# Optimization experiments

Measured on AMD Instinct MI355X. Metric: run time of the kernel, lower is better.

The kernel has to match this reference:

```python
import jax, jax.numpy as jnp
import numpy as np
from jax import lax

B, NM, P, F, E, H, K = 32, 131072, 256, 3, 64, 4, 3
DH = E // H


def layer_norm(x, gamma, beta, eps=1e-5):
    mu = x.mean(-1, keepdims=True)
    var = ((x - mu) ** 2).mean(-1, keepdims=True)
    return (x - mu) * lax.rsqrt(var + eps) * gamma + beta


def knn_interp(x, pos_x, pos_y, k=K):
    """x: [B, Nx, F] features at pos_x [Nx, 2]; interpolate to pos_y [Ny, 2].
    Positions are shared across the batch (they are tiled in the torch code),
    so KNN indices/weights are computed once. Matches torch knn + inverse-
    squared-distance weighted scatter (uniform per-batch counts => gather form).
    """
    d2 = jnp.sum((pos_y[:, None, :] - pos_x[None, :, :]) ** 2, axis=-1)  # [Ny, Nx]
    neg_d2, idx = lax.top_k(-d2, k)                                      # [Ny, k]
    w = 1.0 / jnp.clip(-neg_d2, 1e-16)                                   # [Ny, k]
    w = lax.stop_gradient(w)  # torch computes weights under no_grad
    gathered = x[:, idx, :]                                              # [B, Ny, k, F]
    num = jnp.sum(gathered * w[None, :, :, None], axis=2)                # [B, Ny, F]
    den = jnp.sum(w, axis=1)[None, :, None]                              # [1, Ny, 1]
    return num / den


def setup_inputs() -> dict:
    key = jax.random.key(0)
    ks = jax.random.split(key, 8)
    return {
        "node_attr": jax.random.normal(ks[0], (B * NM, F), jnp.float32),
        "position_mesh": jax.random.uniform(ks[1], (NM, 2), jnp.float32),
        "position_pivotal": jax.random.uniform(ks[2], (P, 2), jnp.float32),
        "ln_gamma": jnp.ones((F,), jnp.float32),
        "ln_beta": jnp.zeros((F,), jnp.float32),
        "Wf": jax.random.normal(ks[3], (E, F), jnp.float32) * (2.0 / E) ** 0.5,
        "bf": jnp.zeros((E,), jnp.float32),
        "Wp": jax.random.normal(ks[4], (E, 2), jnp.float32) * (2.0 / E) ** 0.5,
        "bp": jnp.zeros((E,), jnp.float32),
        "in_proj_w": jax.random.normal(ks[5], (3 * E, E), jnp.float32) * (1.0 / E) ** 0.5,
        "in_proj_b": jnp.zeros((3 * E,), jnp.float32),
        "batch_size": B,
    }


def reference(node_attr, position_mesh, position_pivotal, ln_gamma, ln_beta,
              Wf, bf, Wp, bp, in_proj_w, in_proj_b, batch_size):
    x = node_attr.reshape(batch_size, -1, F)                 # [B, NM, F]
    # PivotalNorm after encoder (encoder/decoder MeshGraphNet omitted: undefined dep)
    x = layer_norm(x, ln_gamma, ln_beta)
    # ---- downsample: mesh -> pivotal via inverse-distance KNN interpolation ----
    y = knn_interp(x, position_mesh, position_pivotal)       # [B, P, F]
    # attention-based pooling over pivotal nodes
    q = (jnp.einsum('bpf,ef->bpe', y, Wf) + bf
         + (position_pivotal @ Wp.T + bp)[None])             # [B, P, E]
    Wq, Wk = in_proj_w[:E], in_proj_w[E:2 * E]
    bq, bk = in_proj_b[:E], in_proj_b[E:2 * E]
    Q = (q @ Wq.T + bq).reshape(batch_size, P, H, DH)
    Kt = (q @ Wk.T + bk).reshape(batch_size, P, H, DH)
    scores = jnp.einsum('bqhd,bkhd->bhqk', Q, Kt) / np.float32(np.sqrt(DH))
    attn = jax.nn.softmax(scores, axis=-1)                   # [B, H, P, P]
    attn_w = attn.mean(axis=1)                               # avg heads, [B, P, P]
    y = jnp.einsum('bqk,bkf->bqf', attn_w, y)                # [B, P, F]
    # ---- interpolate: pivotal -> mesh ----
    out = knn_interp(y, position_pivotal, position_mesh)     # [B, NM, F]
    return out.reshape(-1, F)
```

## Files before the change

### kernel.cpp

```cpp
#include <hip/hip_runtime.h>
#include <math.h>

#define NM 131072
#define PP 256
#define BB 32

#define CHUNKS 512
#define CHUNK_SZ 256

#define INF_F 3.0e38f
#define LDW 13

__device__ __forceinline__ void ins3(float d, int i,
    float& d0, float& d1, float& d2, int& i0, int& i1, int& i2) {
  bool l0 = d < d0, l1 = d < d1, l2 = d < d2;
  d2 = l1 ? d1 : (l2 ? d : d2);
  i2 = l1 ? i1 : (l2 ? i : i2);
  d1 = l0 ? d0 : (l1 ? d : d1);
  i1 = l0 ? i0 : (l1 ? i : i1);
  d0 = l0 ? d : d0;
  i0 = l0 ? i : i0;
}

__device__ __forceinline__ float dist2(float ax, float ay, float bx, float by) {
  float dx = ax - bx, dy = ay - by;
  return __fadd_rn(__fmul_rn(dx, dx), __fmul_rn(dy, dy));
}

__global__ __launch_bounds__(1024)
void knnA_partial(const float* __restrict__ mesh, const float* __restrict__ piv,
                  float* __restrict__ candd, int* __restrict__ candi) {
  const int c = blockIdx.x;
  const int tid = threadIdx.x;
  const int p = tid & 255;
  const int sub = tid >> 8;
  __shared__ float sdf[256 * LDW];
  __shared__ int   sif[256 * LDW];

  const float2 pv = ((const float2*)piv)[p];
  float d0 = INF_F, d1 = INF_F, d2 = INF_F;
  int i0 = 0, i1 = 0, i2 = 0;
  const int base = c * CHUNK_SZ + sub * 64;
#pragma unroll 4
  for (int i = 0; i < 64; ++i) {
    float mx = mesh[2 * (base + i)];
    float my = mesh[2 * (base + i) + 1];
    ins3(dist2(pv.x, pv.y, mx, my), base + i, d0, d1, d2, i0, i1, i2);
  }
  sdf[p * LDW + sub * 3 + 0] = d0; sif[p * LDW + sub * 3 + 0] = i0;
  sdf[p * LDW + sub * 3 + 1] = d1; sif[p * LDW + sub * 3 + 1] = i1;
  sdf[p * LDW + sub * 3 + 2] = d2; sif[p * LDW + sub * 3 + 2] = i2;
  __syncthreads();

  if (tid < 256) {
    float e0 = sdf[tid * LDW + 0], e1 = sdf[tid * LDW + 1], e2 = sdf[tid * LDW + 2];
    int j0 = sif[tid * LDW + 0], j1 = sif[tid * LDW + 1], j2 = sif[tid * LDW + 2];
#pragma unroll
    for (int s = 1; s < 4; ++s)
#pragma unroll
      for (int k = 0; k < 3; ++k)
        ins3(sdf[tid * LDW + s * 3 + k], sif[tid * LDW + s * 3 + k], e0, e1, e2, j0, j1, j2);
    int o = (tid * CHUNKS + c) * 3;
    candd[o] = e0; candd[o + 1] = e1; candd[o + 2] = e2;
    candi[o] = j0; candi[o + 1] = j1; candi[o + 2] = j2;
  }
}

__global__ void knnA_merge(const float* __restrict__ candd, const int* __restrict__ candi,
                           float* __restrict__ wA, int* __restrict__ idxA) {
  const int p = blockIdx.x;
  const int t = threadIdx.x;
  __shared__ float sd[PP * 3];
  __shared__ int si[PP * 3];
  __shared__ float sd2[32 * 3];
  __shared__ int si2[32 * 3];

  float d0 = INF_F, d1 = INF_F, d2 = INF_F;
  int i0 = 0, i1 = 0, i2 = 0;
#pragma unroll
  for (int cc = 0; cc < 2; ++cc) {
    int o = (p * CHUNKS + 2 * t + cc) * 3;
#pragma unroll
    for (int k = 0; k < 3; ++k) ins3(candd[o + k], candi[o + k], d0, d1, d2, i0, i1, i2);
  }
  sd[t * 3] = d0; sd[t * 3 + 1] = d1; sd[t * 3 + 2] = d2;
  si[t * 3] = i0; si[t * 3 + 1] = i1; si[t * 3 + 2] = i2;
  __syncthreads();
  if (t < 32) {
    d0 = d1 = d2 = INF_F; i0 = i1 = i2 = 0;
    for (int j = t * 8; j < t * 8 + 8; ++j)
      for (int k = 0; k < 3; ++k) ins3(sd[j * 3 + k], si[j * 3 + k], d0, d1, d2, i0, i1, i2);
    sd2[t * 3] = d0; sd2[t * 3 + 1] = d1; sd2[t * 3 + 2] = d2;
    si2[t * 3] = i0; si2[t * 3 + 1] = i1; si2[t * 3 + 2] = i2;
  }
  __syncthreads();
  if (t == 0) {
    d0 = d1 = d2 = INF_F; i0 = i1 = i2 = 0;
    for (int j = 0; j < 32; ++j)
      for (int k = 0; k < 3; ++k) ins3(sd2[j * 3 + k], si2[j * 3 + k], d0, d1, d2, i0, i1, i2);
    wA[p * 3 + 0] = 1.0f / fmaxf(d0, 1e-16f); idxA[p * 3 + 0] = i0;
    wA[p * 3 + 1] = 1.0f / fmaxf(d1, 1e-16f); idxA[p * 3 + 1] = i1;
    wA[p * 3 + 2] = 1.0f / fmaxf(d2, 1e-16f); idxA[p * 3 + 2] = i2;
  }
}

__global__ void gather_ln(const float* __restrict__ node, const float* __restrict__ wA,
                          const int* __restrict__ idxA, const float* __restrict__ gamma,
                          const float* __restrict__ beta, float* __restrict__ y) {
  const int b = blockIdx.x >> 2;
  const int p = ((blockIdx.x & 3) << 6) + threadIdx.x;
  const float g0 = gamma[0], g1 = gamma[1], g2 = gamma[2];
  const float be0 = beta[0], be1 = beta[1], be2 = beta[2];
  float num0 = 0.f, num1 = 0.f, num2 = 0.f, den = 0.f;
#pragma unroll
  for (int k = 0; k < 3; ++k) {
    int idx = idxA[p * 3 + k];
    float w = wA[p * 3 + k];
    const float* r = node + ((size_t)b * NM + idx) * 3;
    float a0 = r[0], a1 = r[1], a2 = r[2];
    float mu = (a0 + a1 + a2) * (1.0f / 3.0f);
    float e0 = a0 - mu, e1 = a1 - mu, e2 = a2 - mu;
    float var = (e0 * e0 + e1 * e1 + e2 * e2) * (1.0f / 3.0f);
    float sc = 1.0f / sqrtf(var + 1e-5f);
    float v0 = e0 * sc * g0 + be0, v1 = e1 * sc * g1 + be1, v2 = e2 * sc * g2 + be2;
    num0 += v0 * w; num1 += v1 * w; num2 += v2 * w; den += w;
  }
  int o = (b * PP + p) * 3;
  y[o] = num0 / den; y[o + 1] = num1 / den; y[o + 2] = num2 / den;
}

__global__ __launch_bounds__(128, 2)
void qqk_kernel(const float* __restrict__ y, const float* __restrict__ piv,
                const float* __restrict__ Wf, const float* __restrict__ bf,
                const float* __restrict__ Wp, const float* __restrict__ bp,
                const float* __restrict__ ipw, const float* __restrict__ ipb,
                float* __restrict__ Qh, float* __restrict__ Kh) {
  const int b = blockIdx.x >> 5;
  const int ptile = (blockIdx.x & 31) * 8;
  const int t = threadIdx.x;
  const int e = t & 63;
  const int half = t >> 6;
  __shared__ float qs[8][64];

  {
    float wf0 = Wf[e * 3], wf1 = Wf[e * 3 + 1], wf2 = Wf[e * 3 + 2];
    float wp0 = Wp[e * 2], wp1 = Wp[e * 2 + 1];
    float cst = bf[e] + bp[e];
    for (int r = half; r < 8; r += 2) {
      int p = ptile + r;
      const float* yr = y + (b * PP + p) * 3;
      float pe = piv[2 * p] * wp0 + piv[2 * p + 1] * wp1;
      qs[r][e] = yr[0] * wf0 + yr[1] * wf1 + yr[2] * wf2 + cst + pe;
    }
  }
  __syncthreads();

  const int row = half * 64 + e;
  float wreg[64];
  const float4* W4 = (const float4*)(ipw + row * 64);
#pragma unroll
  for (int j = 0; j < 16; ++j) {
    float4 v = W4[j];
    wreg[4 * j] = v.x; wreg[4 * j + 1] = v.y; wreg[4 * j + 2] = v.z; wreg[4 * j + 3] = v.w;
  }
  float bias = ipb[row];
  float* dst = half ? Kh : Qh;
  const int h = e >> 4, d = e & 15;
  for (int r = 0; r < 8; ++r) {
    float acc = bias;
#pragma unroll
    for (int j = 0; j < 64; ++j) acc += qs[r][j] * wreg[j];
    int p = ptile + r;
    dst[(((b * 4 + h) * PP) + p) * 16 + d] = acc;
  }
}

__global__ void attn_kernel(const float* __restrict__ Qh, const float* __restrict__ Kh,
                            const float* __restrict__ y, float* __restrict__ y2) {
  const int b = blockIdx.x >> 3;
  const int h = (blockIdx.x >> 1) & 3;
  const int qh = blockIdx.x & 1;
  const int t = threadIdx.x;
  const int q = qh * 128 + t;

  __shared__ float Ks[PP * 16];
  __shared__ float ys[PP * 3];

  {
    const float4* src = (const float4*)(Kh + (size_t)(b * 4 + h) * PP * 16);
    float4* dst = (float4*)Ks;
#pragma unroll
    for (int j = 0; j < 8; ++j) dst[j * 128 + t] = src[j * 128 + t];
    const float* ysrc = y + b * PP * 3;
#pragma unroll
    for (int j = 0; j < 6; ++j) ys[j * 128 + t] = ysrc[j * 128 + t];
  }
  __syncthreads();

  const float4* q4 = (const float4*)(Qh + ((size_t)((b * 4 + h) * PP) + q) * 16);
  float4 qa = q4[0], qb = q4[1], qc = q4[2], qd = q4[3];

  float m = -INF_F, l = 0.f, a0 = 0.f, a1 = 0.f, a2 = 0.f;
#pragma unroll 4
  for (int k = 0; k < PP; ++k) {
    const float4* kr = (const float4*)(Ks + k * 16);
    float4 k0 = kr[0], k1 = kr[1], k2 = kr[2], k3 = kr[3];
    float dot = qa.x * k0.x + qa.y * k0.y + qa.z * k0.z + qa.w * k0.w
              + qb.x * k1.x + qb.y * k1.y + qb.z * k1.z + qb.w * k1.w
              + qc.x * k2.x + qc.y * k2.y + qc.z * k2.z + qc.w * k2.w
              + qd.x * k3.x + qd.y * k3.y + qd.z * k3.z + qd.w * k3.w;
    float s = dot * 0.25f;
    float mn = fmaxf(m, s);
    float p = __expf(s - mn);
    float sc = __expf(m - mn);
    float y0 = ys[k * 3], y1 = ys[k * 3 + 1], yy2 = ys[k * 3 + 2];
    l = l * sc + p;
    a0 = a0 * sc + p * y0;
    a1 = a1 * sc + p * y1;
    a2 = a2 * sc + p * yy2;
    m = mn;
  }
  float inv = 0.25f / l;
  float* o = y2 + (b * PP + q) * 3;
  atomicAdd(o + 0, a0 * inv);
  atomicAdd(o + 1, a1 * inv);
  atomicAdd(o + 2, a2 * inv);
}

__global__ __launch_bounds__(256)
void knnB_out(const float* __restrict__ mesh, const float* __restrict__ piv,
              const float* __restrict__ y2, float* __restrict__ out) {
  const int tid = threadIdx.x;
  const int ml = tid & 63;
  const int sub = tid >> 6;
  const int m = blockIdx.x * 64 + ml;
  __shared__ float sdf[64 * LDW];
  __shared__ int   sif[64 * LDW];

  const float2 mv = ((const float2*)mesh)[m];
  float d0 = INF_F, d1 = INF_F, d2 = INF_F;
  int i0 = 0, i1 = 0, i2 = 0;
  const int base = sub * 64;
#pragma unroll 4
  for (int i = 0; i < 64; ++i) {
    int idx = base + i;
    float px = piv[2 * idx], py = piv[2 * idx + 1];
    ins3(dist2(mv.x, mv.y, px, py), idx, d0, d1, d2, i0, i1, i2);
  }
  sdf[ml * LDW + sub * 3 + 0] = d0; sif[ml * LDW + sub * 3 + 0] = i0;
  sdf[ml * LDW + sub * 3 + 1] = d1; sif[ml * LDW + sub * 3 + 1] = i1;
  sdf[ml * LDW + sub * 3 + 2] = d2; sif[ml * LDW + sub * 3 + 2] = i2;
  __syncthreads();

  float e0 = sdf[ml * LDW + 0], e1 = sdf[ml * LDW + 1], e2 = sdf[ml * LDW + 2];
  int j0 = sif[ml * LDW + 0], j1 = sif[ml * LDW + 1], j2 = sif[ml * LDW + 2];
#pragma unroll
  for (int s = 1; s < 4; ++s)
#pragma unroll
    for (int k = 0; k < 3; ++k)
      ins3(sdf[ml * LDW + s * 3 + k], sif[ml * LDW + s * 3 + k], e0, e1, e2, j0, j1, j2);

  float w0 = 1.0f / fmaxf(e0, 1e-16f);
  float w1 = 1.0f / fmaxf(e1, 1e-16f);
  float w2 = 1.0f / fmaxf(e2, 1e-16f);
  float inv = 1.0f / (w0 + w1 + w2);
  const int o0 = j0 * 3, o1 = j1 * 3, o2 = j2 * 3;

#pragma unroll 2
  for (int bi = 0; bi < 8; ++bi) {
    const int b = sub * 8 + bi;
    const float* yb = y2 + b * PP * 3;
    float3 r0 = *(const float3*)(yb + o0);
    float3 r1 = *(const float3*)(yb + o1);
    float3 r2 = *(const float3*)(yb + o2);
    float3 res;
    res.x = (w0 * r0.x + w1 * r1.x + w2 * r2.x) * inv;
    res.y = (w0 * r0.y + w1 * r1.y + w2 * r2.y) * inv;
    res.z = (w0 * r0.z + w1 * r1.z + w2 * r2.z) * inv;
    *(float3*)(out + ((size_t)b * NM + m) * 3) = res;
  }
}

extern "C" void kernel_launch(void* const* d_in, const int* in_sizes, int n_in,
                              void* d_out, int out_size, void* d_ws, size_t ws_size,
                              hipStream_t stream) {
  const float* node  = (const float*)d_in[0];
  const float* mesh  = (const float*)d_in[1];
  const float* piv   = (const float*)d_in[2];
  const float* gamma = (const float*)d_in[3];
  const float* beta  = (const float*)d_in[4];
  const float* Wf    = (const float*)d_in[5];
  const float* bf    = (const float*)d_in[6];
  const float* Wp    = (const float*)d_in[7];
  const float* bp    = (const float*)d_in[8];
  const float* ipw   = (const float*)d_in[9];
  const float* ipb   = (const float*)d_in[10];
  float* out = (float*)d_out;

  float* candd = (float*)d_ws;
  int*   candi = (int*)(candd + CHUNKS * PP * 3);
  float* wA    = (float*)(candi + CHUNKS * PP * 3);
  int*   idxA  = (int*)(wA + PP * 3);
  float* y     = (float*)(idxA + PP * 3);
  float* Qh    = y + BB * PP * 3;
  float* Kh    = Qh + BB * PP * 64;
  float* y2    = Kh + BB * PP * 64;

  hipMemsetAsync(y2, 0, BB * PP * 3 * sizeof(float), stream);

  knnA_partial<<<CHUNKS, 1024, 0, stream>>>(mesh, piv, candd, candi);
  knnA_merge<<<PP, 256, 0, stream>>>(candd, candi, wA, idxA);
  gather_ln<<<BB * 4, 64, 0, stream>>>(node, wA, idxA, gamma, beta, y);
  qqk_kernel<<<BB * 32, 128, 0, stream>>>(y, piv, Wf, bf, Wp, bp, ipw, ipb, Qh, Kh);
  attn_kernel<<<BB * 4 * 2, 128, 0, stream>>>(Qh, Kh, y, y2);
  knnB_out<<<NM / 64, 256, 0, stream>>>(mesh, piv, y2, out);
}
```

Baseline: 212.5 us.

## Fuse KNN-A partial/merge into one kernel and fold gather+LN into qqk

```diff
diff --git a/kernel.cpp b/kernel.cpp
--- a/kernel.cpp
+++ b/kernel.cpp
@@ -4,12 +4,9 @@
 #define NM 131072
 #define PP 256
 #define BB 32
-
-#define CHUNKS 512
-#define CHUNK_SZ 256
-
 #define INF_F 3.0e38f
-#define LDW 13
+
+#define SLOT(x) ((x) + ((x) >> 4))
 
 __device__ __forceinline__ void ins3(float d, int i,
     float& d0, float& d1, float& d2, int& i0, int& i1, int& i2) {
@@ -28,129 +25,130 @@
 }
 
 __global__ __launch_bounds__(1024)
-void knnA_partial(const float* __restrict__ mesh, const float* __restrict__ piv,
-                  float* __restrict__ candd, int* __restrict__ candi) {
-  const int c = blockIdx.x;
-  const int tid = threadIdx.x;
-  const int p = tid & 255;
-  const int sub = tid >> 8;
-  __shared__ float sdf[256 * LDW];
-  __shared__ int   sif[256 * LDW];
-
-  const float2 pv = ((const float2*)piv)[p];
+void knnA_kernel(const float* __restrict__ mesh, const float* __restrict__ piv,
+                 float* __restrict__ wA, int* __restrict__ idxA) {
+  const int p = blockIdx.x;
+  const int t = threadIdx.x;
+  __shared__ float sd0[SLOT(1024)], sd1[SLOT(1024)], sd2[SLOT(1024)];
+  __shared__ int   si0[SLOT(1024)], si1[SLOT(1024)], si2[SLOT(1024)];
+
+  const float px = piv[2 * p], py = piv[2 * p + 1];
   float d0 = INF_F, d1 = INF_F, d2 = INF_F;
   int i0 = 0, i1 = 0, i2 = 0;
-  const int base = c * CHUNK_SZ + sub * 64;
+  const int base = t * 128;
+  const float2* m2 = (const float2*)mesh;
 #pragma unroll 4
-  for (int i = 0; i < 64; ++i) {
-    float mx = mesh[2 * (base + i)];
-    float my = mesh[2 * (base + i) + 1];
-    ins3(dist2(pv.x, pv.y, mx, my), base + i, d0, d1, d2, i0, i1, i2);
-  }
-  sdf[p * LDW + sub * 3 + 0] = d0; sif[p * LDW + sub * 3 + 0] = i0;
-  sdf[p * LDW + sub * 3 + 1] = d1; sif[p * LDW + sub * 3 + 1] = i1;
-  sdf[p * LDW + sub * 3 + 2] = d2; sif[p * LDW + sub * 3 + 2] = i2;
-  __syncthreads();
-
-  if (tid < 256) {
-    float e0 = sdf[tid * LDW + 0], e1 = sdf[tid * LDW + 1], e2 = sdf[tid * LDW + 2];
-    int j0 = sif[tid * LDW + 0], j1 = sif[tid * LDW + 1], j2 = sif[tid * LDW + 2];
-#pragma unroll
-    for (int s = 1; s < 4; ++s)
-#pragma unroll
-      for (int k = 0; k < 3; ++k)
-        ins3(sdf[tid * LDW + s * 3 + k], sif[tid * LDW + s * 3 + k], e0, e1, e2, j0, j1, j2);
-    int o = (tid * CHUNKS + c) * 3;
-    candd[o] = e0; candd[o + 1] = e1; candd[o + 2] = e2;
-    candi[o] = j0; candi[o + 1] = j1; candi[o + 2] = j2;
-  }
-}
-
-__global__ void knnA_merge(const float* __restrict__ candd, const int* __restrict__ candi,
-                           float* __restrict__ wA, int* __restrict__ idxA) {
-  const int p = blockIdx.x;
-  const int t = threadIdx.x;
-  __shared__ float sd[PP * 3];
-  __shared__ int si[PP * 3];
-  __shared__ float sd2[32 * 3];
-  __shared__ int si2[32 * 3];
-
-  float d0 = INF_F, d1 = INF_F, d2 = INF_F;
-  int i0 = 0, i1 = 0, i2 = 0;
-#pragma unroll
-  for (int cc = 0; cc < 2; ++cc) {
-    int o = (p * CHUNKS + 2 * t + cc) * 3;
-#pragma unroll
-    for (int k = 0; k < 3; ++k) ins3(candd[o + k], candi[o + k], d0, d1, d2, i0, i1, i2);
-  }
-  sd[t * 3] = d0; sd[t * 3 + 1] = d1; sd[t * 3 + 2] = d2;
-  si[t * 3] = i0; si[t * 3 + 1] = i1; si[t * 3 + 2] = i2;
-  __syncthreads();
-  if (t < 32) {
+  for (int i = 0; i < 128; ++i) {
+    float2 mv = m2[base + i];
+    ins3(dist2(px, py, mv.x, mv.y), base + i, d0, d1, d2, i0, i1, i2);
+  }
+  sd0[SLOT(t)] = d0; sd1[SLOT(t)] = d1; sd2[SLOT(t)] = d2;
+  si0[SLOT(t)] = i0; si1[SLOT(t)] = i1; si2[SLOT(t)] = i2;
+  __syncthreads();
+
+  if (t < 64) {
     d0 = d1 = d2 = INF_F; i0 = i1 = i2 = 0;
-    for (int j = t * 8; j < t * 8 + 8; ++j)
-      for (int k = 0; k < 3; ++k) ins3(sd[j * 3 + k], si[j * 3 + k], d0, d1, d2, i0, i1, i2);
-    sd2[t * 3] = d0; sd2[t * 3 + 1] = d1; sd2[t * 3 + 2] = d2;
-    si2[t * 3] = i0; si2[t * 3 + 1] = i1; si2[t * 3 + 2] = i2;
-  }
-  __syncthreads();
+    for (int j = t * 16; j < t * 16 + 16; ++j) {
+      int s = SLOT(j);
+      ins3(sd0[s], si0[s], d0, d1, d2, i0, i1, i2);
+      ins3(sd1[s], si1[s], d0, d1, d2, i0, i1, i2);
+      ins3(sd2[s], si2[s], d0, d1, d2, i0, i1, i2);
+    }
+  }
+  __syncthreads();
+  if (t < 64) {
+    sd0[SLOT(t)] = d0; sd1[SLOT(t)] = d1; sd2[SLOT(t)] = d2;
+    si0[SLOT(t)] = i0; si1[SLOT(t)] = i1; si2[SLOT(t)] = i2;
+  }
+  __syncthreads();
+
+  if (t < 8) {
+    d0 = d1 = d2 = INF_F; i0 = i1 = i2 = 0;
+    for (int j = t * 8; j < t * 8 + 8; ++j) {
+      int s = SLOT(j);
+      ins3(sd0[s], si0[s], d0, d1, d2, i0, i1, i2);
+      ins3(sd1[s], si1[s], d0, d1, d2, i0, i1, i2);
+      ins3(sd2[s], si2[s], d0, d1, d2, i0, i1, i2);
+    }
+  }
+  __syncthreads();
+  if (t < 8) {
+    sd0[SLOT(t)] = d0; sd1[SLOT(t)] = d1; sd2[SLOT(t)] = d2;
+    si0[SLOT(t)] = i0; si1[SLOT(t)] = i1; si2[SLOT(t)] = i2;
+  }
+  __syncthreads();
+
   if (t == 0) {
     d0 = d1 = d2 = INF_F; i0 = i1 = i2 = 0;
-    for (int j = 0; j < 32; ++j)
-      for (int k = 0; k < 3; ++k) ins3(sd2[j * 3 + k], si2[j * 3 + k], d0, d1, d2, i0, i1, i2);
+    for (int j = 0; j < 8; ++j) {
+      int s = SLOT(j);
+      ins3(sd0[s], si0[s], d0, d1, d2, i0, i1, i2);
+      ins3(sd1[s], si1[s], d0, d1, d2, i0, i1, i2);
+      ins3(sd2[s], si2[s], d0, d1, d2, i0, i1, i2);
+    }
     wA[p * 3 + 0] = 1.0f / fmaxf(d0, 1e-16f); idxA[p * 3 + 0] = i0;
     wA[p * 3 + 1] = 1.0f / fmaxf(d1, 1e-16f); idxA[p * 3 + 1] = i1;
     wA[p * 3 + 2] = 1.0f / fmaxf(d2, 1e-16f); idxA[p * 3 + 2] = i2;
   }
 }
 
-__global__ void gather_ln(const float* __restrict__ node, const float* __restrict__ wA,
-                          const int* __restrict__ idxA, const float* __restrict__ gamma,
-                          const float* __restrict__ beta, float* __restrict__ y) {
-  const int b = blockIdx.x >> 2;
-  const int p = ((blockIdx.x & 3) << 6) + threadIdx.x;
-  const float g0 = gamma[0], g1 = gamma[1], g2 = gamma[2];
-  const float be0 = beta[0], be1 = beta[1], be2 = beta[2];
-  float num0 = 0.f, num1 = 0.f, num2 = 0.f, den = 0.f;
-#pragma unroll
-  for (int k = 0; k < 3; ++k) {
+__global__ __launch_bounds__(128, 2)
+void qqk_kernel(const float* __restrict__ node, const float* __restrict__ piv,
+                const float* __restrict__ wA, const int* __restrict__ idxA,
+                const float* __restrict__ gamma, const float* __restrict__ beta,
+                const float* __restrict__ Wf, const float* __restrict__ bf,
+                const float* __restrict__ Wp, const float* __restrict__ bp,
+                const float* __restrict__ ipw, const float* __restrict__ ipb,
+                float* __restrict__ y, float* __restrict__ Qh,
+                float* __restrict__ Kh, float* __restrict__ y2) {
+  const int b = blockIdx.x >> 5;
+  const int ptile = (blockIdx.x & 31) * 8;
+  const int t = threadIdx.x;
+  __shared__ float pnum[8][3][3];
+  __shared__ float pden[8][3];
+  __shared__ float ysm[8][3];
+  __shared__ float qs[8][64];
+
+  if (t < 24) {
+    y2[(b * PP + ptile) * 3 + t] = 0.f;
+    int r = t / 3, k = t % 3;
+    int p = ptile + r;
     int idx = idxA[p * 3 + k];
     float w = wA[p * 3 + k];
-    const float* r = node + ((size_t)b * NM + idx) * 3;
-    float a0 = r[0], a1 = r[1], a2 = r[2];
+    const float* rw = node + ((size_t)b * NM + idx) * 3;
+    float a0 = rw[0], a1 = rw[1], a2 = rw[2];
     float mu = (a0 + a1 + a2) * (1.0f / 3.0f);
     float e0 = a0 - mu, e1 = a1 - mu, e2 = a2 - mu;
     float var = (e0 * e0 + e1 * e1 + e2 * e2) * (1.0f / 3.0f);
     float sc = 1.0f / sqrtf(var + 1e-5f);
-    float v0 = e0 * sc * g0 + be0, v1 = e1 * sc * g1 + be1, v2 = e2 * sc * g2 + be2;
-    num0 += v0 * w; num1 += v1 * w; num2 += v2 * w; den += w;
-  }
-  int o = (b * PP + p) * 3;
-  y[o] = num0 / den; y[o + 1] = num1 / den; y[o + 2] = num2 / den;
-}
-
-__global__ __launch_bounds__(128, 2)
-void qqk_kernel(const float* __restrict__ y, const float* __restrict__ piv,
-                const float* __restrict__ Wf, const float* __restrict__ bf,
-                const float* __restrict__ Wp, const float* __restrict__ bp,
-                const float* __restrict__ ipw, const float* __restrict__ ipb,
-                float* __restrict__ Qh, float* __restrict__ Kh) {
-  const int b = blockIdx.x >> 5;
-  const int ptile = (blockIdx.x & 31) * 8;
-  const int t = threadIdx.x;
+    pnum[r][k][0] = (e0 * sc * gamma[0] + beta[0]) * w;
+    pnum[r][k][1] = (e1 * sc * gamma[1] + beta[1]) * w;
+    pnum[r][k][2] = (e2 * sc * gamma[2] + beta[2]) * w;
+    pden[r][k] = w;
+  }
+  __syncthreads();
+  if (t < 8) {
+    float n0 = (pnum[t][0][0] + pnum[t][1][0]) + pnum[t][2][0];
+    float n1 = (pnum[t][0][1] + pnum[t][1][1]) + pnum[t][2][1];
+    float n2 = (pnum[t][0][2] + pnum[t][1][2]) + pnum[t][2][2];
+    float den = (pden[t][0] + pden[t][1]) + pden[t][2];
+    float y0 = n0 / den, y1 = n1 / den, yv2 = n2 / den;
+    ysm[t][0] = y0; ysm[t][1] = y1; ysm[t][2] = yv2;
+    float* yg = y + (b * PP + ptile + t) * 3;
+    yg[0] = y0; yg[1] = y1; yg[2] = yv2;
+  }
+  __syncthreads();
+
   const int e = t & 63;
   const int half = t >> 6;
-  __shared__ float qs[8][64];
-
   {
     float wf0 = Wf[e * 3], wf1 = Wf[e * 3 + 1], wf2 = Wf[e * 3 + 2];
     float wp0 = Wp[e * 2], wp1 = Wp[e * 2 + 1];
     float cst = bf[e] + bp[e];
     for (int r = half; r < 8; r += 2) {
       int p = ptile + r;
-      const float* yr = y + (b * PP + p) * 3;
       float pe = piv[2 * p] * wp0 + piv[2 * p + 1] * wp1;
-      qs[r][e] = yr[0] * wf0 + yr[1] * wf1 + yr[2] * wf2 + cst + pe;
+      qs[r][e] = ysm[r][0] * wf0 + ysm[r][1] * wf1 + ysm[r][2] * wf2 + cst + pe;
     }
   }
   __syncthreads();
@@ -227,6 +225,7 @@
   atomicAdd(o + 2, a2 * inv);
 }
 
+#define LDW 13
 __global__ __launch_bounds__(256)
 void knnB_out(const float* __restrict__ mesh, const float* __restrict__ piv,
               const float* __restrict__ y2, float* __restrict__ out) {
@@ -241,11 +240,12 @@
   float d0 = INF_F, d1 = INF_F, d2 = INF_F;
   int i0 = 0, i1 = 0, i2 = 0;
   const int base = sub * 64;
+  const float2* p2 = (const float2*)piv;
 #pragma unroll 4
   for (int i = 0; i < 64; ++i) {
     int idx = base + i;
-    float px = piv[2 * idx], py = piv[2 * idx + 1];
-    ins3(dist2(mv.x, mv.y, px, py), idx, d0, d1, d2, i0, i1, i2);
+    float2 pv = p2[idx];
+    ins3(dist2(mv.x, mv.y, pv.x, pv.y), idx, d0, d1, d2, i0, i1, i2);
   }
   sdf[ml * LDW + sub * 3 + 0] = d0; sif[ml * LDW + sub * 3 + 0] = i0;
   sdf[ml * LDW + sub * 3 + 1] = d1; sif[ml * LDW + sub * 3 + 1] = i1;
@@ -297,21 +297,16 @@
   const float* ipb   = (const float*)d_in[10];
   float* out = (float*)d_out;
 
-  float* candd = (float*)d_ws;
-  int*   candi = (int*)(candd + CHUNKS * PP * 3);
-  float* wA    = (float*)(candi + CHUNKS * PP * 3);
-  int*   idxA  = (int*)(wA + PP * 3);
-  float* y     = (float*)(idxA + PP * 3);
-  float* Qh    = y + BB * PP * 3;
-  float* Kh    = Qh + BB * PP * 64;
-  float* y2    = Kh + BB * PP * 64;
-
-  hipMemsetAsync(y2, 0, BB * PP * 3 * sizeof(float), stream);
-
-  knnA_partial<<<CHUNKS, 1024, 0, stream>>>(mesh, piv, candd, candi);
-  knnA_merge<<<PP, 256, 0, stream>>>(candd, candi, wA, idxA);
-  gather_ln<<<BB * 4, 64, 0, stream>>>(node, wA, idxA, gamma, beta, y);
-  qqk_kernel<<<BB * 32, 128, 0, stream>>>(y, piv, Wf, bf, Wp, bp, ipw, ipb, Qh, Kh);
+  float* wA   = (float*)d_ws;
+  int*   idxA = (int*)(wA + PP * 3);
+  float* y    = (float*)(idxA + PP * 3);
+  float* Qh   = y + BB * PP * 3;
+  float* Kh   = Qh + BB * PP * 64;
+  float* y2   = Kh + BB * PP * 64;
+
+  knnA_kernel<<<PP, 1024, 0, stream>>>(mesh, piv, wA, idxA);
+  qqk_kernel<<<BB * 32, 128, 0, stream>>>(node, piv, wA, idxA, gamma, beta,
+                                          Wf, bf, Wp, bp, ipw, ipb, y, Qh, Kh, y2);
   attn_kernel<<<BB * 4 * 2, 128, 0, stream>>>(Qh, Kh, y, y2);
   knnB_out<<<NM / 64, 256, 0, stream>>>(mesh, piv, y2, out);
 }
```

Result: no change. 214.7 us (+1.1%).
